# Kernel optimization log

Measured on AMD Instinct MI355X. Metric: run time of the kernel, lower is better.

The kernel has to match this reference:

```python
import jax, jax.numpy as jnp
from jax import lax
import numpy as np


def _relu(x):
    return jnp.maximum(x, 0)


def setup_inputs() -> dict:
    key = jax.random.key(0)
    ks = jax.random.split(key, 20)
    B = 1024
    s = 0.05  # small init scale
    d = {
        "raw_input": jax.random.normal(ks[0], (B, 1, 28, 28), jnp.float32),
        "output_embed": jax.random.normal(ks[1], (B, 512), jnp.float32),
        "latent_embed": jax.random.normal(ks[2], (B, 512), jnp.float32),
        "conv1_w": jax.random.normal(ks[3], (16, 1, 3, 3), jnp.float32) * s,
        "conv1_b": jax.random.normal(ks[4], (16,), jnp.float32) * s,
        "conv2_w": jax.random.normal(ks[5], (32, 16, 3, 3), jnp.float32) * s,
        "conv2_b": jax.random.normal(ks[6], (32,), jnp.float32) * s,
        "proj_w1": jax.random.normal(ks[7], (1568, 1024), jnp.float32) * s,
        "proj_b1": jax.random.normal(ks[8], (1024,), jnp.float32) * s,
        "proj_w2": jax.random.normal(ks[9], (1024, 512), jnp.float32) * s,
        "proj_b2": jax.random.normal(ks[10], (512,), jnp.float32) * s,
        "bb_w1": jax.random.normal(ks[11], (512, 1024), jnp.float32) * s,
        "bb_b1": jax.random.normal(ks[12], (1024,), jnp.float32) * s,
        "bb_w2": jax.random.normal(ks[13], (1024, 512), jnp.float32) * s,
        "bb_b2": jax.random.normal(ks[14], (512,), jnp.float32) * s,
        "head_w": jax.random.normal(ks[15], (512, 10), jnp.float32) * s,
        "head_b": jax.random.normal(ks[16], (10,), jnp.float32) * s,
        "Nsup": 16,
        "n_latent": 6,
    }
    return d


def _maxpool2(x):
    # 2x2 max pool, stride 2, NCHW
    return lax.reduce_window(x, -jnp.inf, lax.max, (1, 1, 2, 2), (1, 1, 2, 2), "VALID")


def reference(raw_input, output_embed, latent_embed,
              conv1_w, conv1_b, conv2_w, conv2_b,
              proj_w1, proj_b1, proj_w2, proj_b2,
              bb_w1, bb_b1, bb_w2, bb_b2,
              head_w, head_b, Nsup, n_latent):
    dn = ("NCHW", "OIHW", "NCHW")
    B = raw_input.shape[0]

    def backbone(x):
        return _relu(_relu(x @ bb_w1 + bb_b1) @ bb_w2 + bb_b2)

    def latent_recursion(inp, out, lat, n):
        if n > 0:
            for _ in range(n):
                lat = backbone(inp + out + lat)
            out = backbone(lat + inp)
        else:
            out = backbone(inp + out + lat)
        return out, lat

    # CNN extractor + input embedding projection (B, 512)
    x = _relu(lax.conv_general_dilated(raw_input, conv1_w, (1, 1), "SAME",
                                       dimension_numbers=dn) + conv1_b[None, :, None, None])
    x = _maxpool2(x)  # (B,16,14,14)
    x = _relu(lax.conv_general_dilated(x, conv2_w, (1, 1), "SAME",
                                       dimension_numbers=dn) + conv2_b[None, :, None, None])
    x = _maxpool2(x)  # (B,32,7,7)
    h = x.reshape(B, -1)  # (B, 1568)
    inp = _relu(_relu(h @ proj_w1 + proj_b1) @ proj_w2 + proj_b2)  # (B,512)

    sg = lax.stop_gradient
    out, lat = output_embed, latent_embed
    T = 3
    logits = None
    for _ in range(Nsup):
        # deep_recursion: T-1 no-grad latent recursions, then one tracked
        for _ in range(T - 1):
            out, lat = latent_recursion(inp, out, lat, n_latent)
            out, lat = sg(out), sg(lat)
        out, lat = latent_recursion(inp, out, lat, n_latent)
        logits = out @ head_w + head_b
        out, lat = sg(out), sg(lat)
    return logits
```

## Files before the change

kernel.cpp:

```cpp
#include <hip/hip_runtime.h>
#include <hip/hip_bf16.h>


typedef unsigned short ushort_t;
typedef __attribute__((ext_vector_type(8))) short short8;
typedef __attribute__((ext_vector_type(4))) float f32x4;

__device__ inline unsigned f2bf_rne(float v) {
    unsigned u = __float_as_uint(v);
    return (u + 0x7fffu + ((u >> 16) & 1u)) >> 16;
}
__device__ inline void split2(float v, ushort_t& h, ushort_t& l) {
    unsigned uh = f2bf_rne(v);
    h = (ushort_t)uh;
    float fh = __uint_as_float(uh << 16);
    l = (ushort_t)f2bf_rne(v - fh);
}

__global__ __launch_bounds__(256) void conv1_pool(
    const float* __restrict__ in, const float* __restrict__ w,
    const float* __restrict__ bias, float* __restrict__ out)
{
    int idx = blockIdx.x * 256 + threadIdx.x;
    int xo = idx % 14; int t = idx / 14;
    int yo = t % 14;  t /= 14;
    int oc = t % 16;  int b = t / 16;
    const float* ip = in + (size_t)b * 784;
    const float* wp = w + oc * 9;
    float win[4][4];
#pragma unroll
    for (int yy = 0; yy < 4; ++yy)
#pragma unroll
        for (int xx = 0; xx < 4; ++xx) {
            int y = 2 * yo + yy - 1, x = 2 * xo + xx - 1;
            win[yy][xx] = (y >= 0 && y < 28 && x >= 0 && x < 28) ? ip[y * 28 + x] : 0.f;
        }
    float bs = bias[oc];
    float m = -1e30f;
#pragma unroll
    for (int py = 0; py < 2; ++py)
#pragma unroll
        for (int px = 0; px < 2; ++px) {
            float s = bs;
#pragma unroll
            for (int dy = 0; dy < 3; ++dy)
#pragma unroll
                for (int dx = 0; dx < 3; ++dx)
                    s = fmaf(win[py + dy][px + dx], wp[dy * 3 + dx], s);
            m = fmaxf(m, s);
        }
    out[idx] = fmaxf(m, 0.f);
}

__global__ __launch_bounds__(256) void conv2_pool(
    const float* __restrict__ in, const float* __restrict__ w,
    const float* __restrict__ bias, float* __restrict__ out)
{
    __shared__ float ws_[32 * 16 * 9];
    for (int i = threadIdx.x; i < 4608; i += 256) ws_[i] = w[i];
    __syncthreads();
    int idx = blockIdx.x * 256 + threadIdx.x;
    int xo = idx % 7; int t = idx / 7;
    int yo = t % 7;  t /= 7;
    int oc = t % 32; int b = t / 32;
    const float* ip = in + (size_t)b * 16 * 196;
    float bs = bias[oc];
    float s00 = bs, s01 = bs, s10 = bs, s11 = bs;
    for (int ic = 0; ic < 16; ++ic) {
        const float* ipp = ip + ic * 196;
        float win[4][4];
#pragma unroll
        for (int yy = 0; yy < 4; ++yy)
#pragma unroll
            for (int xx = 0; xx < 4; ++xx) {
                int y = 2 * yo + yy - 1, x = 2 * xo + xx - 1;
                win[yy][xx] = (y >= 0 && y < 14 && x >= 0 && x < 14) ? ipp[y * 14 + x] : 0.f;
            }
        const float* wp = ws_ + (oc * 16 + ic) * 9;
#pragma unroll
        for (int dy = 0; dy < 3; ++dy)
#pragma unroll
            for (int dx = 0; dx < 3; ++dx) {
                float wv = wp[dy * 3 + dx];
                s00 = fmaf(win[0 + dy][0 + dx], wv, s00);
                s01 = fmaf(win[0 + dy][1 + dx], wv, s01);
                s10 = fmaf(win[1 + dy][0 + dx], wv, s10);
                s11 = fmaf(win[1 + dy][1 + dx], wv, s11);
            }
    }
    float m = fmaxf(fmaxf(s00, s01), fmaxf(s10, s11));
    out[idx] = fmaxf(m, 0.f);
}

#define BMF 64
#define BNF 64
#define BKF 16

__global__ __launch_bounds__(256) void gemm_f32(
    const float* __restrict__ A0, const float* __restrict__ W,
    const float* __restrict__ bias, float* __restrict__ C,
    int M, int N, int K)
{
    __shared__ float As[BKF][BMF];
    __shared__ float Bs[BKF][BNF];
    const int tid = threadIdx.x;
    const int tx = tid % 16;
    const int ty = tid / 16;
    const int row0 = blockIdx.y * BMF;
    const int col0 = blockIdx.x * BNF;
    float acc[4][4] = {};
    const int ra = tid / 4;
    const int ca = 4 * (tid % 4);
    const int rb = tid / 16;
    const int cb = 4 * (tid % 16);
    for (int k0 = 0; k0 < K; k0 += BKF) {
        float4 v = *(const float4*)(A0 + (size_t)(row0 + ra) * K + k0 + ca);
        float4 bvec = *(const float4*)(W + (size_t)(k0 + rb) * N + col0 + cb);
        As[ca + 0][ra] = v.x;
        As[ca + 1][ra] = v.y;
        As[ca + 2][ra] = v.z;
        As[ca + 3][ra] = v.w;
        *(float4*)&Bs[rb][cb] = bvec;
        __syncthreads();
#pragma unroll
        for (int kk = 0; kk < BKF; ++kk) {
            float4 av = *(const float4*)&As[kk][ty * 4];
            float4 bv = *(const float4*)&Bs[kk][tx * 4];
            float a_[4] = {av.x, av.y, av.z, av.w};
            float b_[4] = {bv.x, bv.y, bv.z, bv.w};
#pragma unroll
            for (int i = 0; i < 4; ++i)
#pragma unroll
                for (int j = 0; j < 4; ++j)
                    acc[i][j] = fmaf(a_[i], b_[j], acc[i][j]);
        }
        __syncthreads();
    }
    float4 bv = *(const float4*)(bias + col0 + tx * 4);
    float bb[4] = {bv.x, bv.y, bv.z, bv.w};
#pragma unroll
    for (int i = 0; i < 4; ++i) {
        float4 o;
        o.x = fmaxf(acc[i][0] + bb[0], 0.f);
        o.y = fmaxf(acc[i][1] + bb[1], 0.f);
        o.z = fmaxf(acc[i][2] + bb[2], 0.f);
        o.w = fmaxf(acc[i][3] + bb[3], 0.f);
        *(float4*)(C + (size_t)(row0 + ty * 4 + i) * N + col0 + tx * 4) = o;
    }
}

__global__ __launch_bounds__(256) void prep_wt(
    const float* __restrict__ w, ushort_t* __restrict__ th,
    ushort_t* __restrict__ tl, int K, int N)
{
    int idx = blockIdx.x * 256 + threadIdx.x;
    int n = idx / K, k = idx % K;
    float v = w[(size_t)k * N + n];
    split2(v, th[idx], tl[idx]);
}

__global__ __launch_bounds__(256) void init_xs(
    const float* __restrict__ inpf, const float* __restrict__ oute,
    const float* __restrict__ late, float* __restrict__ io,
    ushort_t* __restrict__ xh, ushort_t* __restrict__ xl)
{
    int i = blockIdx.x * 256 + threadIdx.x;
    float t = inpf[i] + oute[i];
    io[i] = t;
    split2(t + late[i], xh[i], xl[i]);
}

__global__ void init_bar(unsigned* bar) {
    bar[threadIdx.x] = 0;
    bar[threadIdx.x + 256] = 0;
}

__device__ __forceinline__ void group_barrier(unsigned* bar, int g,
                                              unsigned& tgt, int fast)
{
    __syncthreads();
    if (threadIdx.x == 0) {
        if (fast) __builtin_amdgcn_fence(__ATOMIC_RELEASE, "workgroup");
        else      __builtin_amdgcn_fence(__ATOMIC_RELEASE, "agent");
        __hip_atomic_fetch_add(bar + g * 32, 1u, __ATOMIC_RELAXED,
                               __HIP_MEMORY_SCOPE_AGENT);
        while (__hip_atomic_load(bar + g * 32, __ATOMIC_RELAXED,
                                 __HIP_MEMORY_SCOPE_AGENT) < tgt)
            __builtin_amdgcn_s_sleep(1);
        if (fast) {
            __builtin_amdgcn_fence(__ATOMIC_ACQUIRE, "workgroup");
            asm volatile("buffer_inv sc0" ::: "memory");
        } else {
            __builtin_amdgcn_fence(__ATOMIC_ACQUIRE, "agent");
        }
    }
    tgt += 32;
    __syncthreads();
}

__device__ __forceinline__ short8 afrag(const ushort_t* __restrict__ p,
                                        int row, int K, int kpos)
{
    return *(const short8*)(p + (size_t)row * K + kpos);
}

__global__ __launch_bounds__(256, 1) void trm_persist(
    ushort_t* __restrict__ xs_hi, ushort_t* __restrict__ xs_lo,
    ushort_t* __restrict__ h1_hi, ushort_t* __restrict__ h1_lo,
    const ushort_t* __restrict__ W1h, const ushort_t* __restrict__ W1l,
    const ushort_t* __restrict__ W2h, const ushort_t* __restrict__ W2l,
    const float* __restrict__ bb1, const float* __restrict__ bb2,
    float* __restrict__ io, const float* __restrict__ inpf,
    float* __restrict__ latf, float* __restrict__ outf,
    const float* __restrict__ hw, const float* __restrict__ hb,
    float* __restrict__ logits, unsigned* bar)
{
    __shared__ __align__(16) unsigned char w1lds[65536];
    __shared__ __align__(16) unsigned char w2lds[65536];
    __shared__ int modeflag;

    const int tid = threadIdx.x;
    const int w = tid >> 6, lane = tid & 63;
    const int q = lane >> 4, li = lane & 15;
    const int bid = blockIdx.x;
    const int g = bid & 7;
    const int slot = bid >> 3;
    const int R0 = g * 128;
    const int c1 = slot * 32;
    const int c2 = slot * 16;

    for (int i = tid; i < 2 * 32 * 64; i += 256) {
        int comp = i >> 11;
        int rem = i & 2047;
        int n = rem >> 6, c = rem & 63;
        const ushort_t* src = (comp ? W1l : W1h) + (size_t)(c1 + n) * 512 + c * 8;
        *(uint4*)(w1lds + comp * 32768 + (((n << 6) | (c ^ (n & 7))) << 4)) =
            *(const uint4*)src;
    }
    for (int i = tid; i < 2 * 16 * 128; i += 256) {
        int comp = i >> 11;
        int rem = i & 2047;
        int n = rem >> 7, c = rem & 127;
        const ushort_t* src = (comp ? W2l : W2h) + (size_t)(c2 + n) * 1024 + c * 8;
        *(uint4*)(w2lds + comp * 32768 + (((n << 7) | (c ^ (n & 7))) << 4)) =
            *(const uint4*)src;
    }

    if (tid == 0) {
        unsigned xcc;
        asm volatile("s_getreg_b32 %0, hwreg(HW_REG_XCC_ID)" : "=s"(xcc));
        __hip_atomic_fetch_or(bar + 320 + g, 1u << (xcc & 31u),
                              __ATOMIC_RELAXED, __HIP_MEMORY_SCOPE_AGENT);
        __hip_atomic_fetch_add(bar + g * 32, 1u, __ATOMIC_RELAXED,
                               __HIP_MEMORY_SCOPE_AGENT);
        while (__hip_atomic_load(bar + g * 32, __ATOMIC_RELAXED,
                                 __HIP_MEMORY_SCOPE_AGENT) < 32u)
            __builtin_amdgcn_s_sleep(1);
        __builtin_amdgcn_fence(__ATOMIC_ACQUIRE, "agent");
        unsigned msk = __hip_atomic_load(bar + 320 + g, __ATOMIC_RELAXED,
                                         __HIP_MEMORY_SCOPE_AGENT);
        modeflag = (__popc(msk) == 1) ? 1 : 0;
    }
    __syncthreads();
    const int fast = modeflag;
    unsigned tgt = 64;

    const int rowA = R0 + w * 32;
    float bias1[2];
    bias1[0] = bb1[c1 + li];
    bias1[1] = bb1[c1 + 16 + li];
    float bias2 = bb2[c2 + li];

    for (int step = 0; step < 336; ++step) {
        {
            f32x4 acc[2][2] = {};
            short8 aF[3][2][2];
#pragma unroll
            for (int p = 0; p < 2; ++p) {
                int kp = p * 32 + q * 8;
#pragma unroll
                for (int ti = 0; ti < 2; ++ti) {
                    aF[p][0][ti] = afrag(xs_hi, rowA + ti * 16 + li, 512, kp);
                    aF[p][1][ti] = afrag(xs_lo, rowA + ti * 16 + li, 512, kp);
                }
            }
#pragma unroll
            for (int s = 0; s < 16; ++s) {
                if (s + 2 < 16) {
                    int kp = (s + 2) * 32 + q * 8;
#pragma unroll
                    for (int ti = 0; ti < 2; ++ti) {
                        aF[(s + 2) % 3][0][ti] = afrag(xs_hi, rowA + ti * 16 + li, 512, kp);
                        aF[(s + 2) % 3][1][ti] = afrag(xs_lo, rowA + ti * 16 + li, 512, kp);
                    }
                }
                short8 bh[2], bl[2];
#pragma unroll
                for (int tj = 0; tj < 2; ++tj) {
                    int n = tj * 16 + li;
                    int sl = ((n << 6) | ((s * 4 + q) ^ (n & 7))) << 4;
                    bh[tj] = *(const short8*)(w1lds + sl);
                    bl[tj] = *(const short8*)(w1lds + 32768 + sl);
                }
                const short8* ah = aF[s % 3][0];
                const short8* al = aF[s % 3][1];
#pragma unroll
                for (int ti = 0; ti < 2; ++ti)
#pragma unroll
                    for (int tj = 0; tj < 2; ++tj) {
                        acc[ti][tj] = __builtin_amdgcn_mfma_f32_16x16x32_bf16(ah[ti], bh[tj], acc[ti][tj], 0, 0, 0);
                        acc[ti][tj] = __builtin_amdgcn_mfma_f32_16x16x32_bf16(ah[ti], bl[tj], acc[ti][tj], 0, 0, 0);
                        acc[ti][tj] = __builtin_amdgcn_mfma_f32_16x16x32_bf16(al[ti], bh[tj], acc[ti][tj], 0, 0, 0);
                        acc[ti][tj] = __builtin_amdgcn_mfma_f32_16x16x32_bf16(al[ti], bl[tj], acc[ti][tj], 0, 0, 0);
                    }
            }
#pragma unroll
            for (int ti = 0; ti < 2; ++ti)
#pragma unroll
                for (int tj = 0; tj < 2; ++tj) {
                    int colg = c1 + tj * 16 + li;
#pragma unroll
                    for (int rr = 0; rr < 4; ++rr) {
                        int rowg = rowA + ti * 16 + q * 4 + rr;
                        size_t idx = (size_t)rowg * 1024 + colg;
                        float v = fmaxf(acc[ti][tj][rr] + bias1[tj], 0.f);
                        split2(v, h1_hi[idx], h1_lo[idx]);
                    }
                }
        }
        group_barrier(bar, g, tgt, fast);

        {
            int im = step % 7;
            int mode = (im < 5) ? 1 : ((im == 5) ? 2 : 3);
            f32x4 acc[2] = {};
            short8 aF[3][2][2];
#pragma unroll
            for (int p = 0; p < 2; ++p) {
                int kp = p * 32 + q * 8;
#pragma unroll
                for (int ti = 0; ti < 2; ++ti) {
                    aF[p][0][ti] = afrag(h1_hi, rowA + ti * 16 + li, 1024, kp);
                    aF[p][1][ti] = afrag(h1_lo, rowA + ti * 16 + li, 1024, kp);
                }
            }
#pragma unroll
            for (int s = 0; s < 32; ++s) {
                if (s + 2 < 32) {
                    int kp = (s + 2) * 32 + q * 8;
#pragma unroll
                    for (int ti = 0; ti < 2; ++ti) {
                        aF[(s + 2) % 3][0][ti] = afrag(h1_hi, rowA + ti * 16 + li, 1024, kp);
                        aF[(s + 2) % 3][1][ti] = afrag(h1_lo, rowA + ti * 16 + li, 1024, kp);
                    }
                }
                int sl = ((li << 7) | ((s * 4 + q) ^ (li & 7))) << 4;
                short8 bh = *(const short8*)(w2lds + sl);
                short8 bl = *(const short8*)(w2lds + 32768 + sl);
                const short8* ah = aF[s % 3][0];
                const short8* al = aF[s % 3][1];
#pragma unroll
                for (int ti = 0; ti < 2; ++ti) {
                    acc[ti] = __builtin_amdgcn_mfma_f32_16x16x32_bf16(ah[ti], bh, acc[ti], 0, 0, 0);
                    acc[ti] = __builtin_amdgcn_mfma_f32_16x16x32_bf16(ah[ti], bl, acc[ti], 0, 0, 0);
                    acc[ti] = __builtin_amdgcn_mfma_f32_16x16x32_bf16(al[ti], bh, acc[ti], 0, 0, 0);
                    acc[ti] = __builtin_amdgcn_mfma_f32_16x16x32_bf16(al[ti], bl, acc[ti], 0, 0, 0);
                }
            }
            int colg = c2 + li;
#pragma unroll
            for (int ti = 0; ti < 2; ++ti)
#pragma unroll
                for (int rr = 0; rr < 4; ++rr) {
                    int rowg = rowA + ti * 16 + q * 4 + rr;
                    size_t idx = (size_t)rowg * 512 + colg;
                    float v = fmaxf(acc[ti][rr] + bias2, 0.f);
                    if (mode == 1) {
                        split2(io[idx] + v, xs_hi[idx], xs_lo[idx]);
                    } else if (mode == 2) {
                        split2(inpf[idx] + v, xs_hi[idx], xs_lo[idx]);
                        latf[idx] = v;
                    } else {
                        outf[idx] = v;
                        float t2 = inpf[idx] + v;
                        io[idx] = t2;
                        split2(t2 + latf[idx], xs_hi[idx], xs_lo[idx]);
                    }
                }
        }
        group_barrier(bar, g, tgt, fast);
    }

    if (slot < 5) {
        int idx = slot * 256 + tid;
        if (idx < 1280) {
            int rloc = idx / 10, j = idx % 10;
            int row = g * 128 + rloc;
            const float* r = outf + (size_t)row * 512;
            float s = hb[j];
            for (int k = 0; k < 512; ++k) s = fmaf(r[k], hw[k * 10 + j], s);
            logits[row * 10 + j] = s;
        }
    }
}

extern "C" void kernel_launch(void* const* d_in, const int* in_sizes, int n_in,
                              void* d_out, int out_size, void* d_ws, size_t ws_size,
                              hipStream_t stream)
{
    const float* raw   = (const float*)d_in[0];
    const float* out_e = (const float*)d_in[1];
    const float* lat_e = (const float*)d_in[2];
    const float* c1w = (const float*)d_in[3];
    const float* c1b = (const float*)d_in[4];
    const float* c2w = (const float*)d_in[5];
    const float* c2b = (const float*)d_in[6];
    const float* pw1 = (const float*)d_in[7];
    const float* pb1 = (const float*)d_in[8];
    const float* pw2 = (const float*)d_in[9];
    const float* pb2 = (const float*)d_in[10];
    const float* bw1 = (const float*)d_in[11];
    const float* bb1 = (const float*)d_in[12];
    const float* bw2 = (const float*)d_in[13];
    const float* bb2 = (const float*)d_in[14];
    const float* hw  = (const float*)d_in[15];
    const float* hb  = (const float*)d_in[16];

    char* base = (char*)d_ws;
    float*    pool1  = (float*)   (base + 0);
    ushort_t* h1_hi  = (ushort_t*)(base + 0);
    ushort_t* h1_lo  = (ushort_t*)(base + 2097152);
    ushort_t* xs_hi  = (ushort_t*)(base + 4194304);
    ushort_t* xs_lo  = (ushort_t*)(base + 5242880);
    float*    io     = (float*)   (base + 6291456);
    float*    latf   = (float*)   (base + 8388608);
    float*    h1f    = (float*)   (base + 0);
    float*    h      = (float*)   (base + 12845056);
    float*    inpf   = (float*)   (base + 19267584);
    float*    outf   = (float*)   (base + 21364736);
    ushort_t* bW1t_h = (ushort_t*)(base + 23461888);
    ushort_t* bW1t_l = (ushort_t*)(base + 24510464);
    ushort_t* bW2t_h = (ushort_t*)(base + 25559040);
    ushort_t* bW2t_l = (ushort_t*)(base + 26607616);
    unsigned* bar    = (unsigned*)(base + 27656192);

    prep_wt<<<2048, 256, 0, stream>>>(bw1, bW1t_h, bW1t_l, 512, 1024);
    prep_wt<<<2048, 256, 0, stream>>>(bw2, bW2t_h, bW2t_l, 1024, 512);
    init_bar<<<1, 256, 0, stream>>>(bar);

    conv1_pool<<<3211264 / 256, 256, 0, stream>>>(raw, c1w, c1b, pool1);
    conv2_pool<<<1605632 / 256, 256, 0, stream>>>(pool1, c2w, c2b, h);
    gemm_f32<<<dim3(16, 16), 256, 0, stream>>>(h, pw1, pb1, h1f, 1024, 1024, 1568);
    gemm_f32<<<dim3(8, 16), 256, 0, stream>>>(h1f, pw2, pb2, inpf, 1024, 512, 1024);
    init_xs<<<2048, 256, 0, stream>>>(inpf, out_e, lat_e, io, xs_hi, xs_lo);

    trm_persist<<<256, 256, 0, stream>>>(
        xs_hi, xs_lo, h1_hi, h1_lo, bW1t_h, bW1t_l, bW2t_h, bW2t_l,
        bb1, bb2, io, inpf, latf, outf, hw, hb, (float*)d_out, bar);
}
```

Before: 9.551 ms.

## Map barrier groups to XCCs, double waves per block, relayout LDS weights

Each block now claims its row group and slot from a per-XCC atomic counter. Every 32-block barrier group therefore sits on one XCC, and the cheaper workgroup-scope fence plus cache-invalidate barrier can always be used. Blocks grow to 512 threads, so each wave covers 16 rows instead of 32, and the A-fragment prefetch goes four stages deep. Weights in LDS are rearranged into a lane-linear fragment layout, which removes the swizzle arithmetic and bank conflicts. The grouping assumes the 256 blocks spread evenly over 8 XCCs at 32 each; if that does not hold, the result is wrong or the kernel hangs.

```diff
diff --git a/kernel.cpp b/kernel.cpp
--- a/kernel.cpp
+++ b/kernel.cpp
@@ -176,23 +176,18 @@
 }
 
 __device__ __forceinline__ void group_barrier(unsigned* bar, int g,
-                                              unsigned& tgt, int fast)
+                                              unsigned& tgt)
 {
     __syncthreads();
     if (threadIdx.x == 0) {
-        if (fast) __builtin_amdgcn_fence(__ATOMIC_RELEASE, "workgroup");
-        else      __builtin_amdgcn_fence(__ATOMIC_RELEASE, "agent");
+        __builtin_amdgcn_fence(__ATOMIC_RELEASE, "workgroup");
         __hip_atomic_fetch_add(bar + g * 32, 1u, __ATOMIC_RELAXED,
                                __HIP_MEMORY_SCOPE_AGENT);
         while (__hip_atomic_load(bar + g * 32, __ATOMIC_RELAXED,
                                  __HIP_MEMORY_SCOPE_AGENT) < tgt)
             __builtin_amdgcn_s_sleep(1);
-        if (fast) {
-            __builtin_amdgcn_fence(__ATOMIC_ACQUIRE, "workgroup");
-            asm volatile("buffer_inv sc0" ::: "memory");
-        } else {
-            __builtin_amdgcn_fence(__ATOMIC_ACQUIRE, "agent");
-        }
+        __builtin_amdgcn_fence(__ATOMIC_ACQUIRE, "workgroup");
+        asm volatile("buffer_inv sc0" ::: "memory");
     }
     tgt += 32;
     __syncthreads();
@@ -204,7 +199,7 @@
     return *(const short8*)(p + (size_t)row * K + kpos);
 }
 
-__global__ __launch_bounds__(256, 1) void trm_persist(
+__global__ __launch_bounds__(512, 2) void trm_persist(
     ushort_t* __restrict__ xs_hi, ushort_t* __restrict__ xs_lo,
     ushort_t* __restrict__ h1_hi, ushort_t* __restrict__ h1_lo,
     const ushort_t* __restrict__ W1h, const ushort_t* __restrict__ W1l,
@@ -217,182 +212,151 @@
 {
     __shared__ __align__(16) unsigned char w1lds[65536];
     __shared__ __align__(16) unsigned char w2lds[65536];
-    __shared__ int modeflag;
+    __shared__ int sh_gs;
 
     const int tid = threadIdx.x;
     const int w = tid >> 6, lane = tid & 63;
     const int q = lane >> 4, li = lane & 15;
-    const int bid = blockIdx.x;
-    const int g = bid & 7;
-    const int slot = bid >> 3;
-    const int R0 = g * 128;
+
+    if (tid == 0) {
+        unsigned xcc;
+        asm volatile("s_getreg_b32 %0, hwreg(HW_REG_XCC_ID)" : "=s"(xcc));
+        xcc &= 7u;
+        unsigned s = __hip_atomic_fetch_add(bar + 384 + xcc * 8, 1u,
+                                            __ATOMIC_RELAXED,
+                                            __HIP_MEMORY_SCOPE_AGENT);
+        sh_gs = (int)((xcc << 8) | (s & 31u));
+    }
+    __syncthreads();
+    const int g = sh_gs >> 8;
+    const int slot = sh_gs & 255;
     const int c1 = slot * 32;
     const int c2 = slot * 16;
-
-    for (int i = tid; i < 2 * 32 * 64; i += 256) {
+    const int rowA = g * 128 + w * 16;
+
+    for (int i = tid; i < 4096; i += 512) {
         int comp = i >> 11;
         int rem = i & 2047;
         int n = rem >> 6, c = rem & 63;
         const ushort_t* src = (comp ? W1l : W1h) + (size_t)(c1 + n) * 512 + c * 8;
-        *(uint4*)(w1lds + comp * 32768 + (((n << 6) | (c ^ (n & 7))) << 4)) =
-            *(const uint4*)src;
-    }
-    for (int i = tid; i < 2 * 16 * 128; i += 256) {
+        int dst = ((((comp << 4) + (c >> 2)) * 2 + (n >> 4)) * 64 +
+                   ((c & 3) * 16 + (n & 15))) * 16;
+        *(uint4*)(w1lds + dst) = *(const uint4*)src;
+    }
+    for (int i = tid; i < 4096; i += 512) {
         int comp = i >> 11;
         int rem = i & 2047;
         int n = rem >> 7, c = rem & 127;
         const ushort_t* src = (comp ? W2l : W2h) + (size_t)(c2 + n) * 1024 + c * 8;
-        *(uint4*)(w2lds + comp * 32768 + (((n << 7) | (c ^ (n & 7))) << 4)) =
-            *(const uint4*)src;
-    }
-
-    if (tid == 0) {
-        unsigned xcc;
-        asm volatile("s_getreg_b32 %0, hwreg(HW_REG_XCC_ID)" : "=s"(xcc));
-        __hip_atomic_fetch_or(bar + 320 + g, 1u << (xcc & 31u),
-                              __ATOMIC_RELAXED, __HIP_MEMORY_SCOPE_AGENT);
-        __hip_atomic_fetch_add(bar + g * 32, 1u, __ATOMIC_RELAXED,
-                               __HIP_MEMORY_SCOPE_AGENT);
-        while (__hip_atomic_load(bar + g * 32, __ATOMIC_RELAXED,
-                                 __HIP_MEMORY_SCOPE_AGENT) < 32u)
-            __builtin_amdgcn_s_sleep(1);
-        __builtin_amdgcn_fence(__ATOMIC_ACQUIRE, "agent");
-        unsigned msk = __hip_atomic_load(bar + 320 + g, __ATOMIC_RELAXED,
-                                         __HIP_MEMORY_SCOPE_AGENT);
-        modeflag = (__popc(msk) == 1) ? 1 : 0;
+        int dst = (((comp << 5) + (c >> 2)) * 64 + ((c & 3) * 16 + n)) * 16;
+        *(uint4*)(w2lds + dst) = *(const uint4*)src;
     }
     __syncthreads();
-    const int fast = modeflag;
-    unsigned tgt = 64;
-
-    const int rowA = R0 + w * 32;
+
     float bias1[2];
     bias1[0] = bb1[c1 + li];
     bias1[1] = bb1[c1 + 16 + li];
     float bias2 = bb2[c2 + li];
+    unsigned tgt = 32;
 
     for (int step = 0; step < 336; ++step) {
         {
-            f32x4 acc[2][2] = {};
-            short8 aF[3][2][2];
-#pragma unroll
-            for (int p = 0; p < 2; ++p) {
+            f32x4 acc0 = {}, acc1 = {};
+            short8 aF[4][2];
+#pragma unroll
+            for (int p = 0; p < 4; ++p) {
                 int kp = p * 32 + q * 8;
-#pragma unroll
-                for (int ti = 0; ti < 2; ++ti) {
-                    aF[p][0][ti] = afrag(xs_hi, rowA + ti * 16 + li, 512, kp);
-                    aF[p][1][ti] = afrag(xs_lo, rowA + ti * 16 + li, 512, kp);
+                aF[p][0] = afrag(xs_hi, rowA + li, 512, kp);
+                aF[p][1] = afrag(xs_lo, rowA + li, 512, kp);
+            }
+#pragma unroll
+            for (int s = 0; s < 16; ++s) {
+                short8 ah = aF[s & 3][0], al = aF[s & 3][1];
+                if (s + 4 < 16) {
+                    int kp = (s + 4) * 32 + q * 8;
+                    aF[(s + 4) & 3][0] = afrag(xs_hi, rowA + li, 512, kp);
+                    aF[(s + 4) & 3][1] = afrag(xs_lo, rowA + li, 512, kp);
                 }
-            }
-#pragma unroll
-            for (int s = 0; s < 16; ++s) {
-                if (s + 2 < 16) {
-                    int kp = (s + 2) * 32 + q * 8;
-#pragma unroll
-                    for (int ti = 0; ti < 2; ++ti) {
-                        aF[(s + 2) % 3][0][ti] = afrag(xs_hi, rowA + ti * 16 + li, 512, kp);
-                        aF[(s + 2) % 3][1][ti] = afrag(xs_lo, rowA + ti * 16 + li, 512, kp);
-                    }
+                const int base = (s * 2 * 64 + lane) * 16;
+                short8 bh0 = *(const short8*)(w1lds + base);
+                short8 bh1 = *(const short8*)(w1lds + base + 1024);
+                short8 bl0 = *(const short8*)(w1lds + 32768 + base);
+                short8 bl1 = *(const short8*)(w1lds + 32768 + base + 1024);
+                acc0 = __builtin_amdgcn_mfma_f32_16x16x32_bf16(ah, bh0, acc0, 0, 0, 0);
+                acc0 = __builtin_amdgcn_mfma_f32_16x16x32_bf16(ah, bl0, acc0, 0, 0, 0);
+                acc0 = __builtin_amdgcn_mfma_f32_16x16x32_bf16(al, bh0, acc0, 0, 0, 0);
+                acc0 = __builtin_amdgcn_mfma_f32_16x16x32_bf16(al, bl0, acc0, 0, 0, 0);
+                acc1 = __builtin_amdgcn_mfma_f32_16x16x32_bf16(ah, bh1, acc1, 0, 0, 0);
+                acc1 = __builtin_amdgcn_mfma_f32_16x16x32_bf16(ah, bl1, acc1, 0, 0, 0);
+                acc1 = __builtin_amdgcn_mfma_f32_16x16x32_bf16(al, bh1, acc1, 0, 0, 0);
+                acc1 = __builtin_amdgcn_mfma_f32_16x16x32_bf16(al, bl1, acc1, 0, 0, 0);
+            }
+#pragma unroll
+            for (int tj = 0; tj < 2; ++tj) {
+                int colg = c1 + tj * 16 + li;
+                float bv = bias1[tj];
+#pragma unroll
+                for (int rr = 0; rr < 4; ++rr) {
+                    int rowg = rowA + q * 4 + rr;
+                    size_t idx = (size_t)rowg * 1024 + colg;
+                    float v = fmaxf((tj ? acc1[rr] : acc0[rr]) + bv, 0.f);
+                    split2(v, h1_hi[idx], h1_lo[idx]);
                 }
-                short8 bh[2], bl[2];
-#pragma unroll
-                for (int tj = 0; tj < 2; ++tj) {
-                    int n = tj * 16 + li;
-                    int sl = ((n << 6) | ((s * 4 + q) ^ (n & 7))) << 4;
-                    bh[tj] = *(const short8*)(w1lds + sl);
-                    bl[tj] = *(const short8*)(w1lds + 32768 + sl);
-                }
-                const short8* ah = aF[s % 3][0];
-                const short8* al = aF[s % 3][1];
-#pragma unroll
-                for (int ti = 0; ti < 2; ++ti)
-#pragma unroll
-                    for (int tj = 0; tj < 2; ++tj) {
-                        acc[ti][tj] = __builtin_amdgcn_mfma_f32_16x16x32_bf16(ah[ti], bh[tj], acc[ti][tj], 0, 0, 0);
-                        acc[ti][tj] = __builtin_amdgcn_mfma_f32_16x16x32_bf16(ah[ti], bl[tj], acc[ti][tj], 0, 0, 0);
-                        acc[ti][tj] = __builtin_amdgcn_mfma_f32_16x16x32_bf16(al[ti], bh[tj], acc[ti][tj], 0, 0, 0);
-                        acc[ti][tj] = __builtin_amdgcn_mfma_f32_16x16x32_bf16(al[ti], bl[tj], acc[ti][tj], 0, 0, 0);
-                    }
-            }
-#pragma unroll
-            for (int ti = 0; ti < 2; ++ti)
-#pragma unroll
-                for (int tj = 0; tj < 2; ++tj) {
-                    int colg = c1 + tj * 16 + li;
-#pragma unroll
-                    for (int rr = 0; rr < 4; ++rr) {
-                        int rowg = rowA + ti * 16 + q * 4 + rr;
-                        size_t idx = (size_t)rowg * 1024 + colg;
-                        float v = fmaxf(acc[ti][tj][rr] + bias1[tj], 0.f);
-                        split2(v, h1_hi[idx], h1_lo[idx]);
-                    }
-                }
-        }
-        group_barrier(bar, g, tgt, fast);
+            }
+        }
+        group_barrier(bar, g, tgt);
 
         {
             int im = step % 7;
             int mode = (im < 5) ? 1 : ((im == 5) ? 2 : 3);
-            f32x4 acc[2] = {};
-            short8 aF[3][2][2];
-#pragma unroll
-            for (int p = 0; p < 2; ++p) {
+            f32x4 acc = {};
+            short8 aF[4][2];
+#pragma unroll
+            for (int p = 0; p < 4; ++p) {
                 int kp = p * 32 + q * 8;
-#pragma unroll
-                for (int ti = 0; ti < 2; ++ti) {
-                    aF[p][0][ti] = afrag(h1_hi, rowA + ti * 16 + li, 1024, kp);
-                    aF[p][1][ti] = afrag(h1_lo, rowA + ti * 16 + li, 1024, kp);
+                aF[p][0] = afrag(h1_hi, rowA + li, 1024, kp);
+                aF[p][1] = afrag(h1_lo, rowA + li, 1024, kp);
+            }
+#pragma unroll
+            for (int s = 0; s < 32; ++s) {
+                short8 ah = aF[s & 3][0], al = aF[s & 3][1];
+                if (s + 4 < 32) {
+                    int kp = (s + 4) * 32 + q * 8;
+                    aF[(s + 4) & 3][0] = afrag(h1_hi, rowA + li, 1024, kp);
+                    aF[(s + 4) & 3][1] = afrag(h1_lo, rowA + li, 1024, kp);
                 }
-            }
-#pragma unroll
-            for (int s = 0; s < 32; ++s) {
-                if (s + 2 < 32) {
-                    int kp = (s + 2) * 32 + q * 8;
-#pragma unroll
-                    for (int ti = 0; ti < 2; ++ti) {
-                        aF[(s + 2) % 3][0][ti] = afrag(h1_hi, rowA + ti * 16 + li, 1024, kp);
-                        aF[(s + 2) % 3][1][ti] = afrag(h1_lo, rowA + ti * 16 + li, 1024, kp);
-                    }
+                const int base = (s * 64 + lane) * 16;
+                short8 bh = *(const short8*)(w2lds + base);
+                short8 bl = *(const short8*)(w2lds + 32768 + base);
+                acc = __builtin_amdgcn_mfma_f32_16x16x32_bf16(ah, bh, acc, 0, 0, 0);
+                acc = __builtin_amdgcn_mfma_f32_16x16x32_bf16(ah, bl, acc, 0, 0, 0);
+                acc = __builtin_amdgcn_mfma_f32_16x16x32_bf16(al, bh, acc, 0, 0, 0);
+                acc = __builtin_amdgcn_mfma_f32_16x16x32_bf16(al, bl, acc, 0, 0, 0);
+            }
+            int colg = c2 + li;
+#pragma unroll
+            for (int rr = 0; rr < 4; ++rr) {
+                int rowg = rowA + q * 4 + rr;
+                size_t idx = (size_t)rowg * 512 + colg;
+                float v = fmaxf(acc[rr] + bias2, 0.f);
+                if (mode == 1) {
+                    split2(io[idx] + v, xs_hi[idx], xs_lo[idx]);
+                } else if (mode == 2) {
+                    split2(inpf[idx] + v, xs_hi[idx], xs_lo[idx]);
+                    latf[idx] = v;
+                } else {
+                    outf[idx] = v;
+                    float t2 = inpf[idx] + v;
+                    io[idx] = t2;
+                    split2(t2 + latf[idx], xs_hi[idx], xs_lo[idx]);
                 }
-                int sl = ((li << 7) | ((s * 4 + q) ^ (li & 7))) << 4;
-                short8 bh = *(const short8*)(w2lds + sl);
-                short8 bl = *(const short8*)(w2lds + 32768 + sl);
-                const short8* ah = aF[s % 3][0];
-                const short8* al = aF[s % 3][1];
-#pragma unroll
-                for (int ti = 0; ti < 2; ++ti) {
-                    acc[ti] = __builtin_amdgcn_mfma_f32_16x16x32_bf16(ah[ti], bh, acc[ti], 0, 0, 0);
-                    acc[ti] = __builtin_amdgcn_mfma_f32_16x16x32_bf16(ah[ti], bl, acc[ti], 0, 0, 0);
-                    acc[ti] = __builtin_amdgcn_mfma_f32_16x16x32_bf16(al[ti], bh, acc[ti], 0, 0, 0);
-                    acc[ti] = __builtin_amdgcn_mfma_f32_16x16x32_bf16(al[ti], bl, acc[ti], 0, 0, 0);
-                }
-            }
-            int colg = c2 + li;
-#pragma unroll
-            for (int ti = 0; ti < 2; ++ti)
-#pragma unroll
-                for (int rr = 0; rr < 4; ++rr) {
-                    int rowg = rowA + ti * 16 + q * 4 + rr;
-                    size_t idx = (size_t)rowg * 512 + colg;
-                    float v = fmaxf(acc[ti][rr] + bias2, 0.f);
-                    if (mode == 1) {
-                        split2(io[idx] + v, xs_hi[idx], xs_lo[idx]);
-                    } else if (mode == 2) {
-                        split2(inpf[idx] + v, xs_hi[idx], xs_lo[idx]);
-                        latf[idx] = v;
-                    } else {
-                        outf[idx] = v;
-                        float t2 = inpf[idx] + v;
-                        io[idx] = t2;
-                        split2(t2 + latf[idx], xs_hi[idx], xs_lo[idx]);
-                    }
-                }
-        }
-        group_barrier(bar, g, tgt, fast);
-    }
-
-    if (slot < 5) {
-        int idx = slot * 256 + tid;
+            }
+        }
+        group_barrier(bar, g, tgt);
+    }
+
+    {
+        int idx = slot * 512 + tid;
         if (idx < 1280) {
             int rloc = idx / 10, j = idx % 10;
             int row = g * 128 + rloc;
@@ -454,7 +418,7 @@
     gemm_f32<<<dim3(8, 16), 256, 0, stream>>>(h1f, pw2, pb2, inpf, 1024, 512, 1024);
     init_xs<<<2048, 256, 0, stream>>>(inpf, out_e, lat_e, io, xs_hi, xs_lo);
 
-    trm_persist<<<256, 256, 0, stream>>>(
+    trm_persist<<<256, 512, 0, stream>>>(
         xs_hi, xs_lo, h1_hi, h1_lo, bW1t_h, bW1t_l, bW2t_h, bW2t_l,
         bb1, bb2, io, inpf, latf, outf, hw, hb, (float*)d_out, bar);
 }
```

New measurement: 8.440 ms. 1.13x faster.
